# Performance work log

Measured on AMD Instinct MI355X. Metric: run time of the kernel, lower is better.

## Reference

```python
import jax, jax.numpy as jnp
import numpy as np
from jax.scipy.special import logsumexp

B = 2048       # anchors
P = 4          # positives per anchor (constant -> ragged list collapses to [B,P])
D = 256        # embed dim
N_NEG = 32768  # shared negative bank
TEMPERATURE = 0.05
ALPHA = 0.1
EPS = 1e-12    # F.normalize eps


def _l2norm(x):
    n = jnp.sqrt(jnp.sum(x * x, axis=-1, keepdims=True))
    return x / jnp.maximum(n, EPS)


def setup_inputs() -> dict:
    key = jax.random.key(0)
    k1, k2, k3 = jax.random.split(key, 3)
    return {
        "anchor_embeddings": jax.random.normal(k1, (B, D), jnp.float32),
        "positive_embeddings": jax.random.normal(k2, (B * P, D), jnp.float32),
        "negative_embeddings": jax.random.normal(k3, (N_NEG, D), jnp.float32),
        "num_positives_per_anchor": jnp.full((B,), P, dtype=jnp.int32),
    }


def reference(anchor_embeddings, positive_embeddings, negative_embeddings,
              num_positives_per_anchor):
    a = _l2norm(anchor_embeddings)                       # [B, D]
    p = _l2norm(positive_embeddings).reshape(B, P, D)    # [B, P, D]
    n = _l2norm(negative_embeddings)                     # [N, D]

    pos_sim = jnp.einsum("bd,bpd->bp", a, p) / TEMPERATURE   # [B, P]
    neg_sim = jnp.einsum("bd,nd->bn", a, n) / TEMPERATURE    # [B, N]  (dominant traffic)
    neg_lse = logsumexp(neg_sim, axis=1)                     # [B]

    # per-(anchor, positive) CE with label 0 over logits [pos_j, neg_sim_i]:
    # loss = logsumexp([pos_j, neg...]) - pos_j = logaddexp(pos_j, neg_lse_i) - pos_j
    pair_loss = jnp.logaddexp(pos_sim, neg_lse[:, None]) - pos_sim   # [B, P]
    counts = num_positives_per_anchor
    pair_mask = jnp.arange(P)[None, :] < counts[:, None]             # [B, P]
    total = jnp.sum(jnp.where(pair_mask, pair_loss, 0.0))

    # weighted-positive term (only for anchors with num_pos > 1)
    w = jax.nn.softmax(pos_sim, axis=1)                  # [B, P]
    wps = jnp.sum(w * pos_sim, axis=1)                   # [B]
    wloss = jnp.logaddexp(wps, neg_lse) - wps            # [B]
    total = total + ALPHA * jnp.sum(jnp.where(counts > 1, wloss, 0.0))

    return total / B
```

## Files before the change

kernel.cpp:

```cpp
#include <hip/hip_runtime.h>
#include <math.h>

constexpr int   B       = 2048;
constexpr int   P       = 4;
constexpr int   D       = 256;
constexpr int   NNEG    = 32768;
constexpr int   NTILES  = NNEG / 64;
constexpr float TEMP    = 0.05f;
constexpr float ALPHA   = 0.1f;
constexpr float EPS     = 1e-12f;
constexpr float INV_T   = 1.0f / TEMP;
constexpr float SCALE_Q = 28.853900817779268f;

typedef float f32x4 __attribute__((ext_vector_type(4)));
typedef int   i32x8 __attribute__((ext_vector_type(8)));

__device__ inline unsigned short f2bf(float f) {
  unsigned int u = __float_as_uint(f);
  u = (u + 0x7fffu + ((u >> 16) & 1u)) >> 16;
  return (unsigned short)u;
}
__device__ inline float bf2f(unsigned short u) {
  return __uint_as_float((unsigned int)u << 16);
}

__device__ inline float ror16_add(float v) {
  int x;
  x = __builtin_amdgcn_update_dpp(0, __float_as_int(v), 0x121, 0xf, 0xf, true);
  v += __int_as_float(x);
  x = __builtin_amdgcn_update_dpp(0, __float_as_int(v), 0x122, 0xf, 0xf, true);
  v += __int_as_float(x);
  x = __builtin_amdgcn_update_dpp(0, __float_as_int(v), 0x124, 0xf, 0xf, true);
  v += __int_as_float(x);
  x = __builtin_amdgcn_update_dpp(0, __float_as_int(v), 0x128, 0xf, 0xf, true);
  v += __int_as_float(x);
  return v;
}


constexpr int NPANEL = (B + NNEG) / 16;
constexpr int LSTR   = 264;

__global__ __launch_bounds__(256) void prep_kernel(
    const float* __restrict__ a,
    const float* __restrict__ pzx,
    const float* __restrict__ n,
    unsigned char* __restrict__ a_f8,
    unsigned char* __restrict__ n_f8,
    float* __restrict__ pos_sim,
    float* __restrict__ loss_acc,
    unsigned int* __restrict__ ticket) {
  if (blockIdx.x == 0 && threadIdx.x == 0) { *loss_acc = 0.0f; *ticket = 0u; }
  const int id   = blockIdx.x;
  const int tid  = threadIdx.x;
  const int wave = tid >> 6;
  const int lane = tid & 63;

  if (id < NPANEL) {
    __shared__ __align__(16) unsigned short sm[16 * LSTR];
    const float* src; unsigned char* dst; int prow; float post;
    if (id < B / 16) { src = a; dst = a_f8; prow = id;          post = SCALE_Q; }
    else             { src = n; dst = n_f8; prow = id - B / 16; post = 1.0f; }

#pragma unroll
    for (int rr = 0; rr < 4; rr++) {
      const int r = wave * 4 + rr;
      float4 v = ((const float4*)(src + ((size_t)prow * 16 + r) * D))[lane];
      float ss = v.x * v.x + v.y * v.y + v.z * v.z + v.w * v.w;
#pragma unroll
      for (int off = 32; off > 0; off >>= 1) ss += __shfl_xor(ss, off, 64);
      float inv = post / fmaxf(sqrtf(ss), EPS);
      ushort4 o;
      o.x = f2bf(v.x * inv); o.y = f2bf(v.y * inv);
      o.z = f2bf(v.z * inv); o.w = f2bf(v.w * inv);
      *(ushort4*)&sm[r * LSTR + lane * 4] = o;
    }
    __syncthreads();

    const int o  = tid * 16;
    const int r  = (o >> 5) & 15;
    const int k0 = (o >> 11) * 128 + ((o >> 9) & 3) * 32 + (o & 31);
    const unsigned short* s1 = &sm[r * LSTR + k0];
    uint4 ov;
    {
      int w0 = __builtin_amdgcn_cvt_pk_fp8_f32(bf2f(s1[0]),  bf2f(s1[1]),  0,  false);
      w0     = __builtin_amdgcn_cvt_pk_fp8_f32(bf2f(s1[2]),  bf2f(s1[3]),  w0, true);
      int w1 = __builtin_amdgcn_cvt_pk_fp8_f32(bf2f(s1[4]),  bf2f(s1[5]),  0,  false);
      w1     = __builtin_amdgcn_cvt_pk_fp8_f32(bf2f(s1[6]),  bf2f(s1[7]),  w1, true);
      int w2 = __builtin_amdgcn_cvt_pk_fp8_f32(bf2f(s1[8]),  bf2f(s1[9]),  0,  false);
      w2     = __builtin_amdgcn_cvt_pk_fp8_f32(bf2f(s1[10]), bf2f(s1[11]), w2, true);
      int w3 = __builtin_amdgcn_cvt_pk_fp8_f32(bf2f(s1[12]), bf2f(s1[13]), 0,  false);
      w3     = __builtin_amdgcn_cvt_pk_fp8_f32(bf2f(s1[14]), bf2f(s1[15]), w3, true);
      ov.x = (unsigned)w0; ov.y = (unsigned)w1;
      ov.z = (unsigned)w2; ov.w = (unsigned)w3;
    }
    *(uint4*)(dst + (size_t)prow * 4096 + tid * 16) = ov;
  } else {
    int pw = (id - NPANEL) * 4 + wave;
    if (pw >= B * P) return;
    int b = pw >> 2;
    float4 av = ((const float4*)(a + (size_t)b * D))[lane];
    float4 pv = ((const float4*)(pzx + (size_t)pw * D))[lane];
    float d  = av.x * pv.x + av.y * pv.y + av.z * pv.z + av.w * pv.w;
    float sa = av.x * av.x + av.y * av.y + av.z * av.z + av.w * av.w;
    float sp = pv.x * pv.x + pv.y * pv.y + pv.z * pv.z + pv.w * pv.w;
#pragma unroll
    for (int off = 32; off > 0; off >>= 1) {
      d  += __shfl_xor(d, off, 64);
      sa += __shfl_xor(sa, off, 64);
      sp += __shfl_xor(sp, off, 64);
    }
    if (lane == 0) {
      float inva = 1.0f / fmaxf(sqrtf(sa), EPS);
      float invp = 1.0f / fmaxf(sqrtf(sp), EPS);
      pos_sim[pw] = d * inva * invp * INV_T;
    }
  }
}

constexpr int BM = 64, BN = 256;

__global__ __launch_bounds__(512, 4) void negsim_mfma_kernel(
    const unsigned char* __restrict__ Af,
    const unsigned char* __restrict__ Nf,
    float* __restrict__ part_s) {
  __shared__ __align__(16) unsigned char As[4 * 4096];
  __shared__ float part_l[8][64];

  const int tid  = threadIdx.x;
  const int wave = tid >> 6;
  const int lane = tid & 63;

  const int id   = blockIdx.x;
  const int xcd  = id & 7;
  const int j    = id >> 3;
  const int nblk = xcd * 16 + (j & 15);
  const int mblk = j >> 4;
  const int m0   = mblk * BM;
  const int n0   = nblk * BN;

#pragma unroll
  for (int t = 0; t < 2; t++) {
    const int s = wave * 2 + t;
    __builtin_amdgcn_global_load_lds(
        (const __attribute__((address_space(1))) unsigned int*)
            (Af + (size_t)(m0 >> 4) * 4096 + s * 1024 + lane * 16),
        (__attribute__((address_space(3))) unsigned int*)(As + s * 1024 + lane * 16),
        16, 0, 0);
  }

  const unsigned char* Bp = Nf + (size_t)((n0 >> 4) + wave * 2) * 4096 + lane * 32;

  i32x8 bf[2][2];
#pragma unroll
  for (int ni = 0; ni < 2; ni++)
#pragma unroll
    for (int h = 0; h < 2; h++)
      bf[ni][h] = *(const i32x8*)(Bp + (size_t)ni * 4096 + h * 2048);

  __syncthreads();

  f32x4 acc[4][2] = {};

#pragma unroll
  for (int h = 0; h < 2; h++) {
#pragma unroll
    for (int mi = 0; mi < 4; mi++) {
      i32x8 af = *(const i32x8*)&As[mi * 4096 + h * 2048 + lane * 32];
#pragma unroll
      for (int ni = 0; ni < 2; ni++)
        acc[mi][ni] = __builtin_amdgcn_mfma_scale_f32_16x16x128_f8f6f4(
            af, bf[ni][h], acc[mi][ni],
            0, 0,
            0, 0x7f7f7f7f,
            0, 0x7f7f7f7f);
    }
  }

#pragma unroll
  for (int mi = 0; mi < 4; mi++) {
#pragma unroll
    for (int rr = 0; rr < 4; rr++) {
      float e = __builtin_amdgcn_exp2f(acc[mi][0][rr]) +
                __builtin_amdgcn_exp2f(acc[mi][1][rr]);
      e = ror16_add(e);
      if ((lane & 15) == 0)
        part_l[wave][mi * 16 + (lane >> 4) * 4 + rr] = e;
    }
  }
  __syncthreads();
  if (tid < 256) {
    const int u   = tid >> 6;
    const int row = tid & 63;
    float s64 = part_l[2 * u][row] + part_l[2 * u + 1][row];
    part_s[(size_t)(m0 + row) * NTILES + (nblk * 4 + u)] = s64;
  }
}

__global__ void loss_kernel(const float* __restrict__ part_s,
                            const float* __restrict__ pos_sim,
                            const int* __restrict__ counts,
                            float* __restrict__ loss_acc,
                            unsigned int* __restrict__ ticket,
                            float* __restrict__ out) {
  const int tid = threadIdx.x;
  const int b   = blockIdx.x * 16 + (tid >> 4);
  const int sub = tid & 15;
  const float* ps = part_s + (size_t)b * NTILES;
  float s = 0.0f;
#pragma unroll
  for (int i = 0; i < NTILES / 16; i++) s += ps[sub + i * 16];
  s += __shfl_xor(s, 1, 64);
  s += __shfl_xor(s, 2, 64);
  s += __shfl_xor(s, 4, 64);
  s += __shfl_xor(s, 8, 64);

  float acc = 0.0f;
  if (sub == 0) {
    float L = logf(s);
    float p0 = pos_sim[b * P + 0], p1 = pos_sim[b * P + 1];
    float p2 = pos_sim[b * P + 2], p3 = pos_sim[b * P + 3];
    int cnt = counts[b];
    float pj[P] = {p0, p1, p2, p3};
#pragma unroll
    for (int jj = 0; jj < P; jj++) {
      if (jj < cnt) {
        float hi = fmaxf(pj[jj], L), lo = fminf(pj[jj], L);
        acc += hi + log1pf(__expf(lo - hi)) - pj[jj];
      }
    }
    float mp = fmaxf(fmaxf(p0, p1), fmaxf(p2, p3));
    float e0 = __expf(p0 - mp), e1 = __expf(p1 - mp);
    float e2 = __expf(p2 - mp), e3 = __expf(p3 - mp);
    float se = e0 + e1 + e2 + e3;
    float wps = (e0 * p0 + e1 * p1 + e2 * p2 + e3 * p3) / se;
    if (cnt > 1) {
      float hi = fmaxf(wps, L), lo = fminf(wps, L);
      acc += ALPHA * (hi + log1pf(__expf(lo - hi)) - wps);
    }
  }
#pragma unroll
  for (int off = 32; off > 0; off >>= 1) acc += __shfl_xor(acc, off, 64);
  __shared__ float sa[4];
  int wid = tid >> 6, lane = tid & 63;
  if (lane == 0) sa[wid] = acc;
  __syncthreads();
  if (tid == 0) {
    atomicAdd(loss_acc, sa[0] + sa[1] + sa[2] + sa[3]);
    __threadfence();
    unsigned int t = atomicAdd(ticket, 1u);
    if (t == (unsigned int)gridDim.x - 1u) {
      float total = atomicAdd(loss_acc, 0.0f);
      out[0] = total / (float)B;
    }
  }
}

extern "C" void kernel_launch(void* const* d_in, const int* in_sizes, int n_in,
                              void* d_out, int out_size, void* d_ws,
                              size_t ws_size, hipStream_t stream) {
  const float* anc    = (const float*)d_in[0];
  const float* pos    = (const float*)d_in[1];
  const float* neg    = (const float*)d_in[2];
  const int*   counts = (const int*)d_in[3];
  float* out = (float*)d_out;

  unsigned char* a_f8 = (unsigned char*)d_ws;
  unsigned char* n_f8 = a_f8 + (size_t)B * D;
  float* part_s  = (float*)(n_f8 + (size_t)NNEG * D);
  float* pos_sim = part_s + (size_t)B * NTILES;
  float* loss_acc = pos_sim + B * P;
  unsigned int* ticket = (unsigned int*)(loss_acc + 1);

  prep_kernel<<<NPANEL + B * P / 4, 256, 0, stream>>>(
      anc, pos, neg, a_f8, n_f8, pos_sim, loss_acc, ticket);

  negsim_mfma_kernel<<<4096, 512, 0, stream>>>(a_f8, n_f8, part_s);

  loss_kernel<<<B / 16, 256, 0, stream>>>(part_s, pos_sim, counts,
                                          loss_acc, ticket, out);
}
```

Baseline: 121.3 us.

## Make negsim blocks persistent over 8 N tiles with register-resident A

The negsim kernel now launches 512 blocks instead of 4096. Each block keeps its 64-row anchor fragments in registers and loops over 8 negative tiles, loading B fragments directly from global memory. The LDS staging and the cross-wave reduction are gone, and each wave writes its partial sums straight to part_s. This cuts launch and synchronisation overhead and repeated A loads, but it reduces parallelism to 512 blocks, which may leave the GPU underoccupied, and it serialises the B loads within each block.

```diff
diff --git a/kernel.cpp b/kernel.cpp
--- a/kernel.cpp
+++ b/kernel.cpp
@@ -118,82 +118,71 @@
   }
 }
 
-constexpr int BM = 64, BN = 256;
-
 __global__ __launch_bounds__(512, 4) void negsim_mfma_kernel(
     const unsigned char* __restrict__ Af,
     const unsigned char* __restrict__ Nf,
     float* __restrict__ part_s) {
-  __shared__ __align__(16) unsigned char As[4 * 4096];
-  __shared__ float part_l[8][64];
-
-  const int tid  = threadIdx.x;
-  const int wave = tid >> 6;
-  const int lane = tid & 63;
-
-  const int id   = blockIdx.x;
-  const int xcd  = id & 7;
-  const int j    = id >> 3;
-  const int nblk = xcd * 16 + (j & 15);
-  const int mblk = j >> 4;
-  const int m0   = mblk * BM;
-  const int n0   = nblk * BN;
-
-#pragma unroll
-  for (int t = 0; t < 2; t++) {
-    const int s = wave * 2 + t;
-    __builtin_amdgcn_global_load_lds(
-        (const __attribute__((address_space(1))) unsigned int*)
-            (Af + (size_t)(m0 >> 4) * 4096 + s * 1024 + lane * 16),
-        (__attribute__((address_space(3))) unsigned int*)(As + s * 1024 + lane * 16),
-        16, 0, 0);
-  }
-
-  const unsigned char* Bp = Nf + (size_t)((n0 >> 4) + wave * 2) * 4096 + lane * 32;
-
-  i32x8 bf[2][2];
-#pragma unroll
-  for (int ni = 0; ni < 2; ni++)
+  const int tid   = threadIdx.x;
+  const int wave  = tid >> 6;
+  const int lane  = tid & 63;
+  const int mhalf = wave >> 2;
+  const int u     = wave & 3;
+
+  const int id    = blockIdx.x;
+  const int xcd   = id & 7;
+  const int j     = id >> 3;
+  const int mblk  = j >> 1;
+  const int nhalf = j & 1;
+  const int m0    = mblk * 64;
+
+  const unsigned char* Ap =
+      Af + (size_t)((m0 >> 4) + mhalf * 2) * 4096 + lane * 32;
+  i32x8 af[2][2];
+#pragma unroll
+  for (int mi = 0; mi < 2; mi++)
 #pragma unroll
     for (int h = 0; h < 2; h++)
-      bf[ni][h] = *(const i32x8*)(Bp + (size_t)ni * 4096 + h * 2048);
-
-  __syncthreads();
-
-  f32x4 acc[4][2] = {};
-
-#pragma unroll
-  for (int h = 0; h < 2; h++) {
-#pragma unroll
-    for (int mi = 0; mi < 4; mi++) {
-      i32x8 af = *(const i32x8*)&As[mi * 4096 + h * 2048 + lane * 32];
-#pragma unroll
-      for (int ni = 0; ni < 2; ni++)
-        acc[mi][ni] = __builtin_amdgcn_mfma_scale_f32_16x16x128_f8f6f4(
-            af, bf[ni][h], acc[mi][ni],
-            0, 0,
-            0, 0x7f7f7f7f,
-            0, 0x7f7f7f7f);
-    }
-  }
-
-#pragma unroll
-  for (int mi = 0; mi < 4; mi++) {
-#pragma unroll
-    for (int rr = 0; rr < 4; rr++) {
-      float e = __builtin_amdgcn_exp2f(acc[mi][0][rr]) +
-                __builtin_amdgcn_exp2f(acc[mi][1][rr]);
-      e = ror16_add(e);
-      if ((lane & 15) == 0)
-        part_l[wave][mi * 16 + (lane >> 4) * 4 + rr] = e;
-    }
-  }
-  __syncthreads();
-  if (tid < 256) {
-    const int u   = tid >> 6;
-    const int row = tid & 63;
-    float s64 = part_l[2 * u][row] + part_l[2 * u + 1][row];
-    part_s[(size_t)(m0 + row) * NTILES + (nblk * 4 + u)] = s64;
+      af[mi][h] = *(const i32x8*)(Ap + (size_t)mi * 4096 + h * 2048);
+
+  const int row_l = m0 + mhalf * 32 + (lane >> 4) * 4;
+
+#pragma unroll
+  for (int it = 0; it < 8; it++) {
+    const int nblk = xcd * 16 + nhalf * 8 + it;
+    const unsigned char* Bp =
+        Nf + (size_t)(nblk * 16 + u * 4) * 4096 + lane * 32;
+
+    f32x4 acc[2][4] = {};
+#pragma unroll
+    for (int h = 0; h < 2; h++) {
+      i32x8 bf[4];
+#pragma unroll
+      for (int ni = 0; ni < 4; ni++)
+        bf[ni] = *(const i32x8*)(Bp + (size_t)ni * 4096 + h * 2048);
+#pragma unroll
+      for (int mi = 0; mi < 2; mi++)
+#pragma unroll
+        for (int ni = 0; ni < 4; ni++)
+          acc[mi][ni] = __builtin_amdgcn_mfma_scale_f32_16x16x128_f8f6f4(
+              af[mi][h], bf[ni], acc[mi][ni],
+              0, 0,
+              0, 0x7f7f7f7f,
+              0, 0x7f7f7f7f);
+    }
+
+#pragma unroll
+    for (int mi = 0; mi < 2; mi++) {
+#pragma unroll
+      for (int rr = 0; rr < 4; rr++) {
+        float e = __builtin_amdgcn_exp2f(acc[mi][0][rr]) +
+                  __builtin_amdgcn_exp2f(acc[mi][1][rr]) +
+                  __builtin_amdgcn_exp2f(acc[mi][2][rr]) +
+                  __builtin_amdgcn_exp2f(acc[mi][3][rr]);
+        e = ror16_add(e);
+        if ((lane & 15) == 0)
+          part_s[(size_t)(row_l + mi * 16 + rr) * NTILES + (nblk * 4 + u)] = e;
+      }
+    }
   }
 }
 
@@ -275,7 +264,7 @@
   prep_kernel<<<NPANEL + B * P / 4, 256, 0, stream>>>(
       anc, pos, neg, a_f8, n_f8, pos_sim, loss_acc, ticket);
 
-  negsim_mfma_kernel<<<4096, 512, 0, stream>>>(a_f8, n_f8, part_s);
+  negsim_mfma_kernel<<<512, 512, 0, stream>>>(a_f8, n_f8, part_s);
 
   loss_kernel<<<B / 16, 256, 0, stream>>>(part_s, pos_sim, counts,
                                           loss_acc, ticket, out);
```

Measured after the change: 134.5 us. +10.9%, slower.

## Make negsim blocks persistent over eight N tiles with prefetched B fragments

Applied to the files above, without the earlier changes.

The grid drops from 4096 to 512 blocks. Each block keeps its 64-row anchor tile in LDS and loops over 8 negative tiles, so the anchor load and launch overhead are paid once per block instead of per tile. The first-half B fragments for the next tile are loaded while the current tile's second half is computed, giving a software pipeline. In exchange there are fewer blocks (about 2 per CU), two barriers per iteration, and the XCD-aware block mapping is removed, which may reduce occupancy and latency hiding.

```diff
diff --git a/kernel.cpp b/kernel.cpp
--- a/kernel.cpp
+++ b/kernel.cpp
@@ -118,8 +118,6 @@
   }
 }
 
-constexpr int BM = 64, BN = 256;
-
 __global__ __launch_bounds__(512, 4) void negsim_mfma_kernel(
     const unsigned char* __restrict__ Af,
     const unsigned char* __restrict__ Nf,
@@ -131,13 +129,10 @@
   const int wave = tid >> 6;
   const int lane = tid & 63;
 
-  const int id   = blockIdx.x;
-  const int xcd  = id & 7;
-  const int j    = id >> 3;
-  const int nblk = xcd * 16 + (j & 15);
-  const int mblk = j >> 4;
-  const int m0   = mblk * BM;
-  const int n0   = nblk * BN;
+  const int id     = blockIdx.x;
+  const int ngroup = id & 15;
+  const int mblk   = id >> 4;
+  const int m0     = mblk * 64;
 
 #pragma unroll
   for (int t = 0; t < 2; t++) {
@@ -149,51 +144,61 @@
         16, 0, 0);
   }
 
-  const unsigned char* Bp = Nf + (size_t)((n0 >> 4) + wave * 2) * 4096 + lane * 32;
-
-  i32x8 bf[2][2];
-#pragma unroll
-  for (int ni = 0; ni < 2; ni++)
-#pragma unroll
-    for (int h = 0; h < 2; h++)
-      bf[ni][h] = *(const i32x8*)(Bp + (size_t)ni * 4096 + h * 2048);
+  const unsigned char* Bw = Nf + (size_t)(ngroup * 128 + wave * 2) * 4096 + lane * 32;
+
+  i32x8 bfA0 = *(const i32x8*)(Bw);
+  i32x8 bfA1 = *(const i32x8*)(Bw + 4096);
 
   __syncthreads();
 
-  f32x4 acc[4][2] = {};
-
-#pragma unroll
-  for (int h = 0; h < 2; h++) {
+#pragma unroll 1
+  for (int it = 0; it < 8; it++) {
+    const unsigned char* Bp  = Bw + (size_t)it * 16 * 4096;
+    const unsigned char* Bpn = Bw + (size_t)(((it + 1) & 7) * 16) * 4096;
+
+    f32x4 acc[4][2] = {};
+
+    i32x8 bfB0 = *(const i32x8*)(Bp + 2048);
+    i32x8 bfB1 = *(const i32x8*)(Bp + 4096 + 2048);
 #pragma unroll
     for (int mi = 0; mi < 4; mi++) {
-      i32x8 af = *(const i32x8*)&As[mi * 4096 + h * 2048 + lane * 32];
-#pragma unroll
-      for (int ni = 0; ni < 2; ni++)
-        acc[mi][ni] = __builtin_amdgcn_mfma_scale_f32_16x16x128_f8f6f4(
-            af, bf[ni][h], acc[mi][ni],
-            0, 0,
-            0, 0x7f7f7f7f,
-            0, 0x7f7f7f7f);
-    }
-  }
-
-#pragma unroll
-  for (int mi = 0; mi < 4; mi++) {
-#pragma unroll
-    for (int rr = 0; rr < 4; rr++) {
-      float e = __builtin_amdgcn_exp2f(acc[mi][0][rr]) +
-                __builtin_amdgcn_exp2f(acc[mi][1][rr]);
-      e = ror16_add(e);
-      if ((lane & 15) == 0)
-        part_l[wave][mi * 16 + (lane >> 4) * 4 + rr] = e;
-    }
-  }
-  __syncthreads();
-  if (tid < 256) {
-    const int u   = tid >> 6;
-    const int row = tid & 63;
-    float s64 = part_l[2 * u][row] + part_l[2 * u + 1][row];
-    part_s[(size_t)(m0 + row) * NTILES + (nblk * 4 + u)] = s64;
+      i32x8 af = *(const i32x8*)&As[mi * 4096 + lane * 32];
+      acc[mi][0] = __builtin_amdgcn_mfma_scale_f32_16x16x128_f8f6f4(
+          af, bfA0, acc[mi][0], 0, 0, 0, 0x7f7f7f7f, 0, 0x7f7f7f7f);
+      acc[mi][1] = __builtin_amdgcn_mfma_scale_f32_16x16x128_f8f6f4(
+          af, bfA1, acc[mi][1], 0, 0, 0, 0x7f7f7f7f, 0, 0x7f7f7f7f);
+    }
+
+    bfA0 = *(const i32x8*)(Bpn);
+    bfA1 = *(const i32x8*)(Bpn + 4096);
+#pragma unroll
+    for (int mi = 0; mi < 4; mi++) {
+      i32x8 af = *(const i32x8*)&As[mi * 4096 + 2048 + lane * 32];
+      acc[mi][0] = __builtin_amdgcn_mfma_scale_f32_16x16x128_f8f6f4(
+          af, bfB0, acc[mi][0], 0, 0, 0, 0x7f7f7f7f, 0, 0x7f7f7f7f);
+      acc[mi][1] = __builtin_amdgcn_mfma_scale_f32_16x16x128_f8f6f4(
+          af, bfB1, acc[mi][1], 0, 0, 0, 0x7f7f7f7f, 0, 0x7f7f7f7f);
+    }
+
+#pragma unroll
+    for (int mi = 0; mi < 4; mi++) {
+#pragma unroll
+      for (int rr = 0; rr < 4; rr++) {
+        float e = __builtin_amdgcn_exp2f(acc[mi][0][rr]) +
+                  __builtin_amdgcn_exp2f(acc[mi][1][rr]);
+        e = ror16_add(e);
+        if ((lane & 15) == 0)
+          part_l[wave][mi * 16 + (lane >> 4) * 4 + rr] = e;
+      }
+    }
+    __syncthreads();
+    if (tid < 256) {
+      const int u4  = tid >> 6;
+      const int row = tid & 63;
+      float s64 = part_l[2 * u4][row] + part_l[2 * u4 + 1][row];
+      part_s[(size_t)(m0 + row) * NTILES + (ngroup * 32 + it * 4 + u4)] = s64;
+    }
+    __syncthreads();
   }
 }
 
@@ -275,7 +280,7 @@
   prep_kernel<<<NPANEL + B * P / 4, 256, 0, stream>>>(
       anc, pos, neg, a_f8, n_f8, pos_sim, loss_acc, ticket);
 
-  negsim_mfma_kernel<<<4096, 512, 0, stream>>>(a_f8, n_f8, part_s);
+  negsim_mfma_kernel<<<512, 512, 0, stream>>>(a_f8, n_f8, part_s);
 
   loss_kernel<<<B / 16, 256, 0, stream>>>(part_s, pos_sim, counts,
                                           loss_acc, ticket, out);
```

New measurement: 119.8 us. No clear change (-1.2%).
